# Kernel tuning notes

Hardware: AMD Instinct MI355X
Metric: run time of the kernel (lower is better)

The kernel has to match this reference:

```python
import jax, jax.numpy as jnp
import numpy as np

N = 50000      # nodes
E = 800000     # edges
IN = 64        # in_channels
HID = 256      # hidden_dim
LAT = 64       # latent_dim
KS = 2         # kernel_size per dim
DIM = 3        # pseudo-coordinate dim
K = KS ** DIM  # 8 spline weight matrices


def spline_basis_coeffs(pseudo, ks, dim, dtype):
    """Degree-1 open B-spline basis: returns per-edge coefficients c [E, ks**dim]."""
    e = pseudo.shape[0]
    v = pseudo * (ks - 1)                                   # [E, dim]
    bot = jnp.clip(jnp.floor(v), 0, ks - 1).astype(jnp.int32)
    frac = v - bot
    c = jnp.zeros((e, ks ** dim), dtype)
    rows = jnp.arange(e)
    for s in range(2 ** dim):  # 8 knot combinations (fixed small loop)
        w = jnp.ones(e, dtype)
        idx = jnp.zeros(e, jnp.int32)
        for d in range(dim):
            bit = (s >> d) & 1
            w = w * (frac[:, d] if bit else 1.0 - frac[:, d])
            idx = idx + jnp.clip(bot[:, d] + bit, 0, ks - 1) * (ks ** d)
        c = c.at[rows, idx].add(w)
    return c


def spline_conv(x, edge_index, pseudo, W, Wroot, b):
    """SplineConv with aggr='mean', root weight and bias (degree-1 open splines)."""
    src, dst = edge_index[0], edge_index[1]
    n = x.shape[0]
    e = pseudo.shape[0]
    c = spline_basis_coeffs(pseudo, KS, DIM, x.dtype)        # [E, K]
    x_src = x[src]                                           # [E, in] gather
    deg = jax.ops.segment_sum(jnp.ones(e, x.dtype), dst, num_segments=n)
    inv_deg = (1.0 / jnp.maximum(deg, 1.0))[:, None]         # [N, 1] mean aggr
    out = jnp.zeros((n, W.shape[2]), x.dtype)
    for k in range(W.shape[0]):  # K=8 fixed loop; scatter-add then dense matmul
        agg = jax.ops.segment_sum(c[:, k:k + 1] * x_src, dst, num_segments=n)
        out = out + (agg * inv_deg) @ W[k]
    return out + x @ Wroot + b


def setup_inputs() -> dict:
    key = jax.random.key(0)
    ks = jax.random.split(key, 12)
    x = jax.random.normal(ks[0], (N, IN), jnp.float32)
    edge_index = jax.random.randint(ks[1], (2, E), 0, N, jnp.int32)
    s = 0.05
    return {
        "x": x,
        "edge_index": edge_index,
        "conv1_W": jax.random.normal(ks[2], (K, IN, HID), jnp.float32) * s,
        "conv1_root": jax.random.normal(ks[3], (IN, HID), jnp.float32) * s,
        "conv1_b": jnp.zeros((HID,), jnp.float32),
        "conv2_W": jax.random.normal(ks[4], (K, HID, LAT), jnp.float32) * s,
        "conv2_root": jax.random.normal(ks[5], (HID, LAT), jnp.float32) * s,
        "conv2_b": jnp.zeros((LAT,), jnp.float32),
        "dec_w1": jax.random.normal(ks[6], (LAT, HID), jnp.float32) * s,
        "dec_b1": jnp.zeros((HID,), jnp.float32),
        "dec_w2": jax.random.normal(ks[7], (HID, IN), jnp.float32) * s,
        "dec_b2": jnp.zeros((IN,), jnp.float32),
    }


def reference(x, edge_index, conv1_W, conv1_root, conv1_b,
              conv2_W, conv2_root, conv2_b,
              dec_w1, dec_b1, dec_w2, dec_b2):
    pseudo = jnp.zeros((edge_index.shape[1], DIM), x.dtype)  # forward builds zeros
    h = jax.nn.relu(spline_conv(x, edge_index, pseudo, conv1_W, conv1_root, conv1_b))
    z = spline_conv(h, edge_index, pseudo, conv2_W, conv2_root, conv2_b)
    h2 = jax.nn.relu(z @ dec_w1 + dec_b1)
    return h2 @ dec_w2 + dec_b2
```

## Files before the change

kernel.cpp:

```cpp
#include <hip/hip_runtime.h>
#include <hip/hip_bf16.h>


#define THREADS 256

typedef __attribute__((ext_vector_type(8))) short bf16x8;
typedef __attribute__((ext_vector_type(4))) float f32x4;

__device__ __forceinline__ float bf2f(unsigned short u) {
    unsigned v = ((unsigned)u) << 16;
    return __builtin_bit_cast(float, v);
}
__device__ __forceinline__ unsigned short f2bf(float f) {
    __hip_bfloat16 h = __float2bfloat16(f);
    return __builtin_bit_cast(unsigned short, h);
}
__device__ __forceinline__ void acc8(float* f, uint4 v) {
    f[0] += bf2f((unsigned short)v.x); f[1] += bf2f((unsigned short)(v.x >> 16));
    f[2] += bf2f((unsigned short)v.y); f[3] += bf2f((unsigned short)(v.y >> 16));
    f[4] += bf2f((unsigned short)v.z); f[5] += bf2f((unsigned short)(v.z >> 16));
    f[6] += bf2f((unsigned short)v.w); f[7] += bf2f((unsigned short)(v.w >> 16));
}

__device__ __forceinline__ void pack_one(unsigned short* dst,
                                         const float* W0, const float* W1,
                                         int NB, int ksplit, int colsplit,
                                         int ld0, int ld1, int t) {
    int i = t & 7, lane = (t >> 3) & 63, rest = t >> 9;
    int j = rest % NB, s = rest / NB;
    int k = s * 32 + ((lane >> 4) << 3) + i;
    int c = (j << 4) + (lane & 15);
    float v;
    if (c >= colsplit)    v = W1[(size_t)k * ld1 + (c - colsplit)];
    else if (k >= ksplit) v = W1[(size_t)(k - ksplit) * ld1 + c];
    else                  v = W0[(size_t)k * ld0 + c];
    dst[t] = f2bf(v);
}

#define BIG (1 << 30)

__global__ void prep_kernel(const float* __restrict__ W1g, const float* __restrict__ root1,
                            const float* __restrict__ W2g, const float* __restrict__ root2,
                            const float* __restrict__ dw1, const float* __restrict__ dw2,
                            const float* __restrict__ x, const int* __restrict__ dstv,
                            int* __restrict__ bcnt,
                            unsigned short* __restrict__ Pb1,
                            unsigned short* __restrict__ Pb2,
                            unsigned short* __restrict__ Pd1,
                            unsigned short* __restrict__ Pd2,
                            unsigned short* __restrict__ ab1,
                            int n, int E, int pb_pack) {
    if ((int)blockIdx.x >= pb_pack) {
        __shared__ int hist[256];
        int t = threadIdx.x;
        hist[t] = 0;
        __syncthreads();
        int e0 = ((int)blockIdx.x - pb_pack) * 4096;
#pragma unroll
        for (int i = 0; i < 16; ++i) {
            int e = e0 + t + i * 256;
            if (e < E) atomicAdd(&hist[dstv[e] >> 8], 1);
        }
        __syncthreads();
        int h = hist[t];
        if (h) atomicAdd(&bcnt[t], h);
        return;
    }
    int t = blockIdx.x * blockDim.x + threadIdx.x;
    if (t < 32768) {
        pack_one(Pb1, W1g, root1, 16, 64, BIG, 256, 256, t);
    } else if (t < 65536) {
        pack_one(Pb2, W2g, root2, 8, BIG, 64, 64, 64, t - 32768);
    } else if (t < 81920) {
        pack_one(Pd1, dw1, dw1, 16, BIG, BIG, 256, 256, t - 65536);
    } else if (t < 98304) {
        pack_one(Pd2, dw2, dw2, 4, BIG, BIG, 64, 64, t - 81920);
    } else if (t < 98304 + n * 16) {
        int u = t - 98304;
        int row = u >> 4, c4 = (u & 15) * 4;
        float4 v = *(const float4*)(x + (size_t)row * 64 + c4);
        unsigned lo = (unsigned)f2bf(v.x) | ((unsigned)f2bf(v.y) << 16);
        unsigned hi = (unsigned)f2bf(v.z) | ((unsigned)f2bf(v.w) << 16);
        uint2 o; o.x = lo; o.y = hi;
        *(uint2*)(ab1 + (size_t)row * 128 + 64 + c4) = o;
    }
}

__global__ __launch_bounds__(512) void partition_edges(
    const int* __restrict__ src, const int* __restrict__ dst,
    const int* __restrict__ bcnt, int* __restrict__ bcur,
    int* __restrict__ epack, int E) {
    __shared__ int hist[256];
    __shared__ int base[256];
    __shared__ int lcur[256];
    __shared__ int bb[256];
    int t = threadIdx.x;
    if (t < 256) { hist[t] = 0; lcur[t] = 0; }
    __syncthreads();
    int e0 = blockIdx.x * 2048;
    int myd[4], mys[4];
#pragma unroll
    for (int i = 0; i < 4; ++i) {
        int e = e0 + t + i * 512;
        int d = (e < E) ? dst[e] : -1;
        mys[i] = (e < E) ? src[e] : 0;
        myd[i] = d;
        if (d >= 0) atomicAdd(&hist[d >> 8], 1);
    }
    int cb = 0;
    if (t < 256) { cb = bcnt[t]; bb[t] = cb; }
    __syncthreads();
    for (int off = 1; off < 256; off <<= 1) {
        int xv = (t >= off && t < 256) ? bb[t - off] : 0;
        __syncthreads();
        if (t < 256) bb[t] += xv;
        __syncthreads();
    }
    if (t < 256) {
        int h = hist[t];
        if (h > 0) base[t] = (bb[t] - cb) + atomicAdd(&bcur[t], h);
    }
    __syncthreads();
#pragma unroll
    for (int i = 0; i < 4; ++i) {
        int d = myd[i];
        if (d >= 0) {
            int b = d >> 8;
            int p = atomicAdd(&lcur[b], 1);
            epack[base[b] + p] = ((d & 255) << 20) | mys[i];
        }
    }
}

__global__ __launch_bounds__(1024) void bucket_fill2(
    const int* __restrict__ epack, const int* __restrict__ bcnt,
    int* __restrict__ offs, float* __restrict__ invd,
    int* __restrict__ esrc, int N) {
    __shared__ int sb_[256];
    __shared__ int nh[256];
    __shared__ int loff[256];
    __shared__ int ncur[256];
    __shared__ int stage[8192];
    int b = blockIdx.x, t = threadIdx.x;
    int n0 = b << 8;
    int cb = 0;
    if (t < 256) { cb = bcnt[t]; sb_[t] = cb; }
    __syncthreads();
    for (int off = 1; off < 256; off <<= 1) {
        int xv = (t >= off && t < 256) ? sb_[t - off] : 0;
        __syncthreads();
        if (t < 256) sb_[t] += xv;
        __syncthreads();
    }
    int ebase = b ? sb_[b - 1] : 0;
    int ecount = sb_[b] - ebase;
    if (b == 0 && t == 0) offs[N] = sb_[255];
    if (t < 256) nh[t] = 0;
    __syncthreads();
    for (int i = t; i < ecount; i += 1024)
        atomicAdd(&nh[epack[ebase + i] >> 20], 1);
    __syncthreads();
    int v = 0;
    if (t < 256) { v = nh[t]; loff[t] = v; }
    __syncthreads();
    for (int off = 1; off < 256; off <<= 1) {
        int xv = (t >= off && t < 256) ? loff[t - off] : 0;
        __syncthreads();
        if (t < 256) loff[t] += xv;
        __syncthreads();
    }
    if (t < 256) {
        int ex = loff[t] - v;
        loff[t] = ex;
        int node = n0 + t;
        if (node < N) {
            offs[node] = ebase + ex;
            invd[node] = 1.0f / (float)max(v, 1);
        }
        ncur[t] = 0;
    }
    __syncthreads();
    bool useLds = (ecount <= 8192);
    for (int i = t; i < ecount; i += 1024) {
        int p = epack[ebase + i];
        int dl = p >> 20;
        int pos = atomicAdd(&ncur[dl], 1);
        int g = loff[dl] + pos;
        int sv = p & 0xFFFFF;
        if (useLds) stage[g] = sv;
        else        esrc[ebase + g] = sv;
    }
    __syncthreads();
    if (useLds)
        for (int i = t; i < ecount; i += 1024) esrc[ebase + i] = stage[i];
}

__global__ void agg_x4(unsigned short* __restrict__ ab1, const int* __restrict__ esrc,
                       const int* __restrict__ offs, const float* __restrict__ invd,
                       int n) {
    int node = blockIdx.x * 4 + (threadIdx.x >> 6);
    if (node >= n) return;
    int l = threadIdx.x & 63;
    int slot = l >> 3, c = l & 7;
    const unsigned short* xb = ab1 + 64 + c * 8;
    int s = offs[node], e = offs[node + 1];
    float a0[8] = {}, a1[8] = {};
    int j = s;
    for (; j + 16 <= e; j += 16) {
        int i0 = esrc[j + slot], i1 = esrc[j + 8 + slot];
        uint4 v0 = *(const uint4*)(xb + (size_t)i0 * 128);
        uint4 v1 = *(const uint4*)(xb + (size_t)i1 * 128);
        acc8(a0, v0); acc8(a1, v1);
    }
    if (j + 8 <= e) {
        int i0 = esrc[j + slot];
        uint4 v0 = *(const uint4*)(xb + (size_t)i0 * 128);
        acc8(a0, v0);
        j += 8;
    }
    if (slot < e - j) {
        int i0 = esrc[j + slot];
        uint4 v0 = *(const uint4*)(xb + (size_t)i0 * 128);
        acc8(a1, v0);
    }
    float r[8];
#pragma unroll
    for (int k = 0; k < 8; ++k) {
        r[k] = a0[k] + a1[k];
        r[k] += __shfl_xor(r[k], 8);
        r[k] += __shfl_xor(r[k], 16);
        r[k] += __shfl_xor(r[k], 32);
    }
    if (slot == 0) {
        float iv = invd[node];
        unsigned p0 = (unsigned)f2bf(r[0] * iv) | ((unsigned)f2bf(r[1] * iv) << 16);
        unsigned p1 = (unsigned)f2bf(r[2] * iv) | ((unsigned)f2bf(r[3] * iv) << 16);
        unsigned p2 = (unsigned)f2bf(r[4] * iv) | ((unsigned)f2bf(r[5] * iv) << 16);
        unsigned p3 = (unsigned)f2bf(r[6] * iv) | ((unsigned)f2bf(r[7] * iv) << 16);
        uint4 o; o.x = p0; o.y = p1; o.z = p2; o.w = p3;
        *(uint4*)(ab1 + (size_t)node * 128 + c * 8) = o;
    }
}

__global__ void agg_z4(const unsigned short* __restrict__ hwroot,
                       const int* __restrict__ esrc, const int* __restrict__ offs,
                       const float* __restrict__ invd, const float* __restrict__ b2,
                       unsigned short* __restrict__ z, int n) {
    int node = blockIdx.x * 4 + (threadIdx.x >> 6);
    if (node >= n) return;
    int l = threadIdx.x & 63;
    int slot = l >> 3, c = l & 7;
    const unsigned short* hb = hwroot + c * 8;
    int s = offs[node], e = offs[node + 1];
    float a0[8] = {}, a1[8] = {};
    int j = s;
    for (; j + 16 <= e; j += 16) {
        int i0 = esrc[j + slot], i1 = esrc[j + 8 + slot];
        uint4 v0 = *(const uint4*)(hb + (size_t)i0 * 128);
        uint4 v1 = *(const uint4*)(hb + (size_t)i1 * 128);
        acc8(a0, v0); acc8(a1, v1);
    }
    if (j + 8 <= e) {
        int i0 = esrc[j + slot];
        uint4 v0 = *(const uint4*)(hb + (size_t)i0 * 128);
        acc8(a0, v0);
        j += 8;
    }
    if (slot < e - j) {
        int i0 = esrc[j + slot];
        uint4 v0 = *(const uint4*)(hb + (size_t)i0 * 128);
        acc8(a1, v0);
    }
    float r[8];
#pragma unroll
    for (int k = 0; k < 8; ++k) {
        r[k] = a0[k] + a1[k];
        r[k] += __shfl_xor(r[k], 8);
        r[k] += __shfl_xor(r[k], 16);
        r[k] += __shfl_xor(r[k], 32);
    }
    if (slot == 0) {
        float iv = invd[node];
        uint4 hr = *(const uint4*)(hwroot + (size_t)node * 128 + 64 + c * 8);
        float4 bA = *(const float4*)(b2 + c * 8);
        float4 bB = *(const float4*)(b2 + c * 8 + 4);
        float v0 = r[0] * iv + bf2f((unsigned short)hr.x) + bA.x;
        float v1 = r[1] * iv + bf2f((unsigned short)(hr.x >> 16)) + bA.y;
        float v2 = r[2] * iv + bf2f((unsigned short)hr.y) + bA.z;
        float v3 = r[3] * iv + bf2f((unsigned short)(hr.y >> 16)) + bA.w;
        float v4 = r[4] * iv + bf2f((unsigned short)hr.z) + bB.x;
        float v5 = r[5] * iv + bf2f((unsigned short)(hr.z >> 16)) + bB.y;
        float v6 = r[6] * iv + bf2f((unsigned short)hr.w) + bB.z;
        float v7 = r[7] * iv + bf2f((unsigned short)(hr.w >> 16)) + bB.w;
        unsigned p0 = (unsigned)f2bf(v0) | ((unsigned)f2bf(v1) << 16);
        unsigned p1 = (unsigned)f2bf(v2) | ((unsigned)f2bf(v3) << 16);
        unsigned p2 = (unsigned)f2bf(v4) | ((unsigned)f2bf(v5) << 16);
        unsigned p3 = (unsigned)f2bf(v6) | ((unsigned)f2bf(v7) << 16);
        uint4 o; o.x = p0; o.y = p1; o.z = p2; o.w = p3;
        *(uint4*)(z + (size_t)node * 64 + c * 8) = o;
    }
}

template <int K1, int NBW2, bool OUTBF>
__global__ __launch_bounds__(256) void gemm_fused(
    const unsigned short* __restrict__ A,
    const unsigned short* __restrict__ Bp1, const float* __restrict__ bias1,
    const unsigned short* __restrict__ Bp2, const float* __restrict__ bias2,
    void* __restrict__ Cv, int n)
{
    constexpr int KS1 = K1 / 32;
    constexpr int N2 = NBW2 * 64;
    constexpr int NB2 = NBW2 * 4;
    __shared__ unsigned short ht[64][264];

    const int m0 = blockIdx.x * 64;
    const int lane = threadIdx.x & 63;
    const int w = threadIdx.x >> 6;
    const int quad = lane >> 4;
    const int l16 = lane & 15;

    {
        f32x4 acc[4][4] = {};
        const unsigned short* Arow = A + (size_t)(m0 + l16) * K1 + quad * 8;
        for (int s = 0; s < KS1; ++s) {
            bf16x8 a[4];
#pragma unroll
            for (int mb = 0; mb < 4; ++mb)
                a[mb] = *(const bf16x8*)(Arow + (size_t)mb * 16 * K1 + s * 32);
#pragma unroll
            for (int jn = 0; jn < 4; ++jn) {
                int j = w * 4 + jn;
                bf16x8 b = *(const bf16x8*)(Bp1 + ((size_t)(s * 16 + j) * 64 + lane) * 8);
#pragma unroll
                for (int mb = 0; mb < 4; ++mb)
                    acc[mb][jn] = __builtin_amdgcn_mfma_f32_16x16x32_bf16(a[mb], b, acc[mb][jn], 0, 0, 0);
            }
        }
#pragma unroll
        for (int jn = 0; jn < 4; ++jn) {
            int col = (w * 4 + jn) * 16 + l16;
            float bv = bias1[col];
#pragma unroll
            for (int mb = 0; mb < 4; ++mb)
#pragma unroll
                for (int r = 0; r < 4; ++r) {
                    int row = mb * 16 + quad * 4 + r;
                    ht[row][col] = f2bf(fmaxf(acc[mb][jn][r] + bv, 0.f));
                }
        }
    }
    __syncthreads();

    {
        f32x4 acc[4][NBW2] = {};
        for (int s = 0; s < 8; ++s) {
            bf16x8 a[4];
#pragma unroll
            for (int mb = 0; mb < 4; ++mb)
                a[mb] = *(const bf16x8*)&ht[mb * 16 + l16][s * 32 + quad * 8];
#pragma unroll
            for (int jn = 0; jn < NBW2; ++jn) {
                int j = w * NBW2 + jn;
                bf16x8 b = *(const bf16x8*)(Bp2 + ((size_t)(s * NB2 + j) * 64 + lane) * 8);
#pragma unroll
                for (int mb = 0; mb < 4; ++mb)
                    acc[mb][jn] = __builtin_amdgcn_mfma_f32_16x16x32_bf16(a[mb], b, acc[mb][jn], 0, 0, 0);
            }
        }
#pragma unroll
        for (int jn = 0; jn < NBW2; ++jn) {
            int col = (w * NBW2 + jn) * 16 + l16;
            float bv = bias2 ? bias2[col] : 0.f;
#pragma unroll
            for (int mb = 0; mb < 4; ++mb)
#pragma unroll
                for (int r = 0; r < 4; ++r) {
                    int row = m0 + mb * 16 + quad * 4 + r;
                    if (row < n) {
                        float v = acc[mb][jn][r] + bv;
                        if (OUTBF)
                            ((unsigned short*)Cv)[(size_t)row * N2 + col] = f2bf(v);
                        else
                            ((float*)Cv)[(size_t)row * N2 + col] = v;
                    }
                }
        }
    }
}

extern "C" void kernel_launch(void* const* d_in, const int* in_sizes, int n_in,
                              void* d_out, int out_size, void* d_ws, size_t ws_size,
                              hipStream_t stream) {
    const float* x      = (const float*)d_in[0];
    const int*   ei     = (const int*)d_in[1];
    const float* W1g    = (const float*)d_in[2];
    const float* root1  = (const float*)d_in[3];
    const float* b1     = (const float*)d_in[4];
    const float* W2g    = (const float*)d_in[5];
    const float* root2  = (const float*)d_in[6];
    const float* b2     = (const float*)d_in[7];
    const float* dw1    = (const float*)d_in[8];
    const float* db1    = (const float*)d_in[9];
    const float* dw2    = (const float*)d_in[10];
    const float* db2    = (const float*)d_in[11];
    float* out = (float*)d_out;

    const int N = in_sizes[0] / 64;
    const int E = in_sizes[1] / 2;
    const int Npad = N + 64;
    const int* srcv = ei;
    const int* dstv = ei + E;

    char* ws = (char*)d_ws;
    auto alloc = [&](size_t bytes) -> void* {
        void* p = (void*)ws;
        ws += (bytes + 255) & ~(size_t)255;
        return p;
    };
    int*   bcnt   = (int*)alloc(1024);
    int*   bcur   = (int*)alloc(1024);
    int*   offs   = (int*)alloc((size_t)(N + 1) * 4);
    float* invd   = (float*)alloc((size_t)N * 4);
    int*   esrc   = (int*)alloc((size_t)E * 4);
    int*   epack  = (int*)alloc((size_t)E * 4);
    unsigned short* Pb1 = (unsigned short*)alloc(32768 * 2);
    unsigned short* Pb2 = (unsigned short*)alloc(32768 * 2);
    unsigned short* Pd1 = (unsigned short*)alloc(16384 * 2);
    unsigned short* Pd2 = (unsigned short*)alloc(16384 * 2);
    unsigned short* ab1    = (unsigned short*)alloc((size_t)Npad * 128 * 2);
    unsigned short* hwroot = (unsigned short*)alloc((size_t)Npad * 128 * 2);
    unsigned short* z      = (unsigned short*)alloc((size_t)Npad * 64 * 2);

    hipMemsetAsync(bcnt, 0, 2048, stream);

    int gb = (N + 63) / 64;
    int nbkt = (N + 255) / 256;
    int pa = (E + 4095) / 4096;
    int pa2 = (E + 2047) / 2048;
    int pb_pack = (98304 + N * 16 + THREADS - 1) / THREADS;

    prep_kernel<<<pb_pack + pa, THREADS, 0, stream>>>(
        W1g, root1, W2g, root2, dw1, dw2, x, dstv, bcnt,
        Pb1, Pb2, Pd1, Pd2, ab1, N, E, pb_pack);
    partition_edges<<<pa2, 512, 0, stream>>>(srcv, dstv, bcnt, bcur, epack, E);
    bucket_fill2<<<nbkt, 1024, 0, stream>>>(epack, bcnt, offs, invd, esrc, N);

    agg_x4<<<(N + 3) / 4, THREADS, 0, stream>>>(ab1, esrc, offs, invd, N);
    gemm_fused<128, 2, true><<<gb, 256, 0, stream>>>(ab1, Pb1, b1, Pb2, nullptr, hwroot, N);
    agg_z4<<<(N + 3) / 4, THREADS, 0, stream>>>(hwroot, esrc, offs, invd, b2, z, N);
    gemm_fused<64, 1, false><<<gb, 256, 0, stream>>>(z, Pd1, db1, Pd2, db2, out, N);
}
```

Measured before the change: 198.0 us.

## Split neighbor aggregation into per-feature-slice blocks for cache locality

Replaces the per-node aggregation kernels with a templated kernel in which each block handles one 16-byte feature slice (8 bf16 values) for 32 nodes. Consecutive blocks walk the same nodes across different slices, and each gather touches only one 16B slice of a 256B row. The intent is a smaller working set per slice so gathered rows stay in L2/MALL. Each wave now handles 4 nodes at once with 16 edge slots per node and a divergent __any loop. The histogram pass in prep also uses 2048-edge chunks to match partition_edges, adding more parallelism.

```diff
diff --git a/kernel.cpp b/kernel.cpp
--- a/kernel.cpp
+++ b/kernel.cpp
@@ -55,9 +55,9 @@
         int t = threadIdx.x;
         hist[t] = 0;
         __syncthreads();
-        int e0 = ((int)blockIdx.x - pb_pack) * 4096;
-#pragma unroll
-        for (int i = 0; i < 16; ++i) {
+        int e0 = ((int)blockIdx.x - pb_pack) * 2048;
+#pragma unroll
+        for (int i = 0; i < 8; ++i) {
             int e = e0 + t + i * 256;
             if (e < E) atomicAdd(&hist[dstv[e] >> 8], 1);
         }
@@ -195,109 +195,66 @@
         for (int i = t; i < ecount; i += 1024) esrc[ebase + i] = stage[i];
 }
 
-__global__ void agg_x4(unsigned short* __restrict__ ab1, const int* __restrict__ esrc,
-                       const int* __restrict__ offs, const float* __restrict__ invd,
-                       int n) {
-    int node = blockIdx.x * 4 + (threadIdx.x >> 6);
-    if (node >= n) return;
-    int l = threadIdx.x & 63;
-    int slot = l >> 3, c = l & 7;
-    const unsigned short* xb = ab1 + 64 + c * 8;
-    int s = offs[node], e = offs[node + 1];
-    float a0[8] = {}, a1[8] = {};
-    int j = s;
-    for (; j + 16 <= e; j += 16) {
-        int i0 = esrc[j + slot], i1 = esrc[j + 8 + slot];
-        uint4 v0 = *(const uint4*)(xb + (size_t)i0 * 128);
-        uint4 v1 = *(const uint4*)(xb + (size_t)i1 * 128);
-        acc8(a0, v0); acc8(a1, v1);
-    }
-    if (j + 8 <= e) {
-        int i0 = esrc[j + slot];
-        uint4 v0 = *(const uint4*)(xb + (size_t)i0 * 128);
-        acc8(a0, v0);
-        j += 8;
-    }
-    if (slot < e - j) {
-        int i0 = esrc[j + slot];
-        uint4 v0 = *(const uint4*)(xb + (size_t)i0 * 128);
-        acc8(a1, v0);
-    }
-    float r[8];
-#pragma unroll
-    for (int k = 0; k < 8; ++k) {
-        r[k] = a0[k] + a1[k];
-        r[k] += __shfl_xor(r[k], 8);
-        r[k] += __shfl_xor(r[k], 16);
-        r[k] += __shfl_xor(r[k], 32);
-    }
-    if (slot == 0) {
-        float iv = invd[node];
-        unsigned p0 = (unsigned)f2bf(r[0] * iv) | ((unsigned)f2bf(r[1] * iv) << 16);
-        unsigned p1 = (unsigned)f2bf(r[2] * iv) | ((unsigned)f2bf(r[3] * iv) << 16);
-        unsigned p2 = (unsigned)f2bf(r[4] * iv) | ((unsigned)f2bf(r[5] * iv) << 16);
-        unsigned p3 = (unsigned)f2bf(r[6] * iv) | ((unsigned)f2bf(r[7] * iv) << 16);
-        uint4 o; o.x = p0; o.y = p1; o.z = p2; o.w = p3;
-        *(uint4*)(ab1 + (size_t)node * 128 + c * 8) = o;
-    }
-}
-
-__global__ void agg_z4(const unsigned short* __restrict__ hwroot,
-                       const int* __restrict__ esrc, const int* __restrict__ offs,
-                       const float* __restrict__ invd, const float* __restrict__ b2,
-                       unsigned short* __restrict__ z, int n) {
-    int node = blockIdx.x * 4 + (threadIdx.x >> 6);
-    if (node >= n) return;
-    int l = threadIdx.x & 63;
-    int slot = l >> 3, c = l & 7;
-    const unsigned short* hb = hwroot + c * 8;
-    int s = offs[node], e = offs[node + 1];
-    float a0[8] = {}, a1[8] = {};
-    int j = s;
-    for (; j + 16 <= e; j += 16) {
-        int i0 = esrc[j + slot], i1 = esrc[j + 8 + slot];
-        uint4 v0 = *(const uint4*)(hb + (size_t)i0 * 128);
-        uint4 v1 = *(const uint4*)(hb + (size_t)i1 * 128);
-        acc8(a0, v0); acc8(a1, v1);
-    }
-    if (j + 8 <= e) {
-        int i0 = esrc[j + slot];
-        uint4 v0 = *(const uint4*)(hb + (size_t)i0 * 128);
-        acc8(a0, v0);
-        j += 8;
-    }
-    if (slot < e - j) {
-        int i0 = esrc[j + slot];
-        uint4 v0 = *(const uint4*)(hb + (size_t)i0 * 128);
-        acc8(a1, v0);
-    }
-    float r[8];
-#pragma unroll
-    for (int k = 0; k < 8; ++k) {
-        r[k] = a0[k] + a1[k];
-        r[k] += __shfl_xor(r[k], 8);
-        r[k] += __shfl_xor(r[k], 16);
-        r[k] += __shfl_xor(r[k], 32);
-    }
-    if (slot == 0) {
-        float iv = invd[node];
-        uint4 hr = *(const uint4*)(hwroot + (size_t)node * 128 + 64 + c * 8);
-        float4 bA = *(const float4*)(b2 + c * 8);
-        float4 bB = *(const float4*)(b2 + c * 8 + 4);
-        float v0 = r[0] * iv + bf2f((unsigned short)hr.x) + bA.x;
-        float v1 = r[1] * iv + bf2f((unsigned short)(hr.x >> 16)) + bA.y;
-        float v2 = r[2] * iv + bf2f((unsigned short)hr.y) + bA.z;
-        float v3 = r[3] * iv + bf2f((unsigned short)(hr.y >> 16)) + bA.w;
-        float v4 = r[4] * iv + bf2f((unsigned short)hr.z) + bB.x;
-        float v5 = r[5] * iv + bf2f((unsigned short)(hr.z >> 16)) + bB.y;
-        float v6 = r[6] * iv + bf2f((unsigned short)hr.w) + bB.z;
-        float v7 = r[7] * iv + bf2f((unsigned short)(hr.w >> 16)) + bB.w;
-        unsigned p0 = (unsigned)f2bf(v0) | ((unsigned)f2bf(v1) << 16);
-        unsigned p1 = (unsigned)f2bf(v2) | ((unsigned)f2bf(v3) << 16);
-        unsigned p2 = (unsigned)f2bf(v4) | ((unsigned)f2bf(v5) << 16);
-        unsigned p3 = (unsigned)f2bf(v6) | ((unsigned)f2bf(v7) << 16);
-        uint4 o; o.x = p0; o.y = p1; o.z = p2; o.w = p3;
-        *(uint4*)(z + (size_t)node * 64 + c * 8) = o;
+template <int MODE>
+__global__ __launch_bounds__(256) void agg_slice(
+    const unsigned short* __restrict__ tbl,
+    const int* __restrict__ esrc, const int* __restrict__ offs,
+    const float* __restrict__ invd, const float* __restrict__ b2,
+    const unsigned short* __restrict__ hwroot,
+    unsigned short* __restrict__ outb, int n) {
+    const int b = blockIdx.x;
+    const int s = b & 7, grp = b >> 3;
+    const int l = threadIdx.x & 63, w = threadIdx.x >> 6;
+    const int nsub = l & 3, slot = l >> 2;
+    const int OS = (MODE == 0) ? 128 : 64;
+    const unsigned short* tb = tbl + ((MODE == 0) ? 64 : 0) + s * 8;
+
+#pragma unroll
+    for (int q = 0; q < 2; ++q) {
+        int node = grp * 32 + w * 8 + q * 4 + nsub;
+        bool valid = node < n;
+        int s0 = valid ? offs[node] : 0;
+        int e0 = valid ? offs[node + 1] : 0;
+        float a[8] = {};
+        int j = s0 + slot;
+        while (__any(j < e0)) {
+            if (j < e0) {
+                int src = esrc[j];
+                uint4 v = *(const uint4*)(tb + (size_t)src * 128);
+                acc8(a, v);
+            }
+            j += 16;
+        }
+#pragma unroll
+        for (int k = 0; k < 8; ++k) {
+            a[k] += __shfl_xor(a[k], 4);
+            a[k] += __shfl_xor(a[k], 8);
+            a[k] += __shfl_xor(a[k], 16);
+            a[k] += __shfl_xor(a[k], 32);
+        }
+        if (slot == 0 && valid) {
+            float iv = invd[node];
+            float v[8];
+#pragma unroll
+            for (int k = 0; k < 8; ++k) v[k] = a[k] * iv;
+            if (MODE == 1) {
+                uint4 hr = *(const uint4*)(hwroot + (size_t)node * 128 + 64 + s * 8);
+                v[0] += bf2f((unsigned short)hr.x)         + b2[s * 8 + 0];
+                v[1] += bf2f((unsigned short)(hr.x >> 16)) + b2[s * 8 + 1];
+                v[2] += bf2f((unsigned short)hr.y)         + b2[s * 8 + 2];
+                v[3] += bf2f((unsigned short)(hr.y >> 16)) + b2[s * 8 + 3];
+                v[4] += bf2f((unsigned short)hr.z)         + b2[s * 8 + 4];
+                v[5] += bf2f((unsigned short)(hr.z >> 16)) + b2[s * 8 + 5];
+                v[6] += bf2f((unsigned short)hr.w)         + b2[s * 8 + 6];
+                v[7] += bf2f((unsigned short)(hr.w >> 16)) + b2[s * 8 + 7];
+            }
+            unsigned p0 = (unsigned)f2bf(v[0]) | ((unsigned)f2bf(v[1]) << 16);
+            unsigned p1 = (unsigned)f2bf(v[2]) | ((unsigned)f2bf(v[3]) << 16);
+            unsigned p2 = (unsigned)f2bf(v[4]) | ((unsigned)f2bf(v[5]) << 16);
+            unsigned p3 = (unsigned)f2bf(v[6]) | ((unsigned)f2bf(v[7]) << 16);
+            uint4 o; o.x = p0; o.y = p1; o.z = p2; o.w = p3;
+            *(uint4*)(outb + (size_t)node * OS + s * 8) = o;
+        }
     }
 }
 
@@ -435,18 +392,20 @@
 
     int gb = (N + 63) / 64;
     int nbkt = (N + 255) / 256;
-    int pa = (E + 4095) / 4096;
-    int pa2 = (E + 2047) / 2048;
+    int pa = (E + 2047) / 2048;
     int pb_pack = (98304 + N * 16 + THREADS - 1) / THREADS;
+    int ga = ((N + 31) / 32) * 8;
 
     prep_kernel<<<pb_pack + pa, THREADS, 0, stream>>>(
         W1g, root1, W2g, root2, dw1, dw2, x, dstv, bcnt,
         Pb1, Pb2, Pd1, Pd2, ab1, N, E, pb_pack);
-    partition_edges<<<pa2, 512, 0, stream>>>(srcv, dstv, bcnt, bcur, epack, E);
+    partition_edges<<<pa, 512, 0, stream>>>(srcv, dstv, bcnt, bcur, epack, E);
     bucket_fill2<<<nbkt, 1024, 0, stream>>>(epack, bcnt, offs, invd, esrc, N);
 
-    agg_x4<<<(N + 3) / 4, THREADS, 0, stream>>>(ab1, esrc, offs, invd, N);
+    agg_slice<0><<<ga, THREADS, 0, stream>>>(ab1, esrc, offs, invd, nullptr,
+                                             nullptr, ab1, N);
     gemm_fused<128, 2, true><<<gb, 256, 0, stream>>>(ab1, Pb1, b1, Pb2, nullptr, hwroot, N);
-    agg_z4<<<(N + 3) / 4, THREADS, 0, stream>>>(hwroot, esrc, offs, invd, b2, z, N);
+    agg_slice<1><<<ga, THREADS, 0, stream>>>(hwroot, esrc, offs, invd, b2,
+                                             hwroot, z, N);
     gemm_fused<64, 1, false><<<gb, 256, 0, stream>>>(z, Pd1, db1, Pd2, db2, out, N);
 }
```

Result: slower. 297.4 us (+50.2%).

## Split LDS histograms into four sub-bins and reuse atomic ranks for scatter

Applied to the files above, without the earlier changes.

The bucket histograms in prep, partition and bucket_fill are spread across four sub-bins per bucket, picked by lane index, so fewer lanes contend on the same LDS atomic. The rank returned by the first atomic is kept and combined with a scan over the sub-bins to place each edge directly. This replaces the second atomic pass and the LDS staging buffer. In exchange it adds a 1024-entry prefix scan per block and more LDS use, and the esrc writes become scattered global stores rather than a coalesced copy from LDS.

```diff
diff --git a/kernel.cpp b/kernel.cpp
--- a/kernel.cpp
+++ b/kernel.cpp
@@ -51,18 +51,19 @@
                             unsigned short* __restrict__ ab1,
                             int n, int E, int pb_pack) {
     if ((int)blockIdx.x >= pb_pack) {
-        __shared__ int hist[256];
+        __shared__ int hist[1024];
         int t = threadIdx.x;
-        hist[t] = 0;
+        hist[t] = 0; hist[t + 256] = 0; hist[t + 512] = 0; hist[t + 768] = 0;
         __syncthreads();
         int e0 = ((int)blockIdx.x - pb_pack) * 4096;
+        int sub = t & 3;
 #pragma unroll
         for (int i = 0; i < 16; ++i) {
             int e = e0 + t + i * 256;
-            if (e < E) atomicAdd(&hist[dstv[e] >> 8], 1);
-        }
-        __syncthreads();
-        int h = hist[t];
+            if (e < E) atomicAdd(&hist[((dstv[e] >> 8) << 2) | sub], 1);
+        }
+        __syncthreads();
+        int h = hist[t * 4] + hist[t * 4 + 1] + hist[t * 4 + 2] + hist[t * 4 + 3];
         if (h) atomicAdd(&bcnt[t], h);
         return;
     }
@@ -90,22 +91,33 @@
     const int* __restrict__ src, const int* __restrict__ dst,
     const int* __restrict__ bcnt, int* __restrict__ bcur,
     int* __restrict__ epack, int E) {
-    __shared__ int hist[256];
+    __shared__ int h4[1024];
+    __shared__ int s4[1024];
     __shared__ int base[256];
-    __shared__ int lcur[256];
     __shared__ int bb[256];
     int t = threadIdx.x;
-    if (t < 256) { hist[t] = 0; lcur[t] = 0; }
+    h4[t] = 0; h4[t + 512] = 0;
     __syncthreads();
     int e0 = blockIdx.x * 2048;
-    int myd[4], mys[4];
+    int sub = t & 3;
+    int myd[4], mys[4], myr[4];
 #pragma unroll
     for (int i = 0; i < 4; ++i) {
         int e = e0 + t + i * 512;
         int d = (e < E) ? dst[e] : -1;
         mys[i] = (e < E) ? src[e] : 0;
         myd[i] = d;
-        if (d >= 0) atomicAdd(&hist[d >> 8], 1);
+        if (d >= 0) myr[i] = atomicAdd(&h4[((d >> 8) << 2) | sub], 1);
+    }
+    __syncthreads();
+    s4[t] = h4[t]; s4[t + 512] = h4[t + 512];
+    __syncthreads();
+    for (int off = 1; off < 1024; off <<= 1) {
+        int v0 = (t >= off) ? s4[t - off] : 0;
+        int v1 = (t + 512 >= off) ? s4[t + 512 - off] : 0;
+        __syncthreads();
+        s4[t] += v0; s4[t + 512] += v1;
+        __syncthreads();
     }
     int cb = 0;
     if (t < 256) { cb = bcnt[t]; bb[t] = cb; }
@@ -117,8 +129,10 @@
         __syncthreads();
     }
     if (t < 256) {
-        int h = hist[t];
-        if (h > 0) base[t] = (bb[t] - cb) + atomicAdd(&bcur[t], h);
+        int lo = t ? s4[t * 4 - 1] : 0;
+        int h = s4[t * 4 + 3] - lo;
+        if (h > 0)
+            base[t] = (bb[t] - cb) + atomicAdd(&bcur[t], h) - lo;
     }
     __syncthreads();
 #pragma unroll
@@ -126,8 +140,9 @@
         int d = myd[i];
         if (d >= 0) {
             int b = d >> 8;
-            int p = atomicAdd(&lcur[b], 1);
-            epack[base[b] + p] = ((d & 255) << 20) | mys[i];
+            int flat = (b << 2) | sub;
+            int pre = flat ? s4[flat - 1] : 0;
+            epack[base[b] + pre + myr[i]] = ((d & 255) << 20) | mys[i];
         }
     }
 }
@@ -137,10 +152,9 @@
     int* __restrict__ offs, float* __restrict__ invd,
     int* __restrict__ esrc, int N) {
     __shared__ int sb_[256];
-    __shared__ int nh[256];
-    __shared__ int loff[256];
+    __shared__ int n4[1024];
     __shared__ int ncur[256];
-    __shared__ int stage[8192];
+    __shared__ int rk[8192];
     int b = blockIdx.x, t = threadIdx.x;
     int n0 = b << 8;
     int cb = 0;
@@ -155,44 +169,50 @@
     int ebase = b ? sb_[b - 1] : 0;
     int ecount = sb_[b] - ebase;
     if (b == 0 && t == 0) offs[N] = sb_[255];
-    if (t < 256) nh[t] = 0;
-    __syncthreads();
-    for (int i = t; i < ecount; i += 1024)
-        atomicAdd(&nh[epack[ebase + i] >> 20], 1);
-    __syncthreads();
-    int v = 0;
-    if (t < 256) { v = nh[t]; loff[t] = v; }
-    __syncthreads();
-    for (int off = 1; off < 256; off <<= 1) {
-        int xv = (t >= off && t < 256) ? loff[t - off] : 0;
-        __syncthreads();
-        if (t < 256) loff[t] += xv;
+    n4[t] = 0;
+    __syncthreads();
+    bool useRk = (ecount <= 8192);
+    int sub = t & 3;
+    for (int i = t; i < ecount; i += 1024) {
+        int dl = epack[ebase + i] >> 20;
+        int r = atomicAdd(&n4[(dl << 2) | sub], 1);
+        if (useRk) rk[i] = r;
+    }
+    __syncthreads();
+    for (int off = 1; off < 1024; off <<= 1) {
+        int xv = (t >= off) ? n4[t - off] : 0;
+        __syncthreads();
+        n4[t] += xv;
         __syncthreads();
     }
     if (t < 256) {
-        int ex = loff[t] - v;
-        loff[t] = ex;
+        int lo = t ? n4[t * 4 - 1] : 0;
+        int v = n4[t * 4 + 3] - lo;
         int node = n0 + t;
         if (node < N) {
-            offs[node] = ebase + ex;
+            offs[node] = ebase + lo;
             invd[node] = 1.0f / (float)max(v, 1);
         }
         ncur[t] = 0;
     }
     __syncthreads();
-    bool useLds = (ecount <= 8192);
-    for (int i = t; i < ecount; i += 1024) {
-        int p = epack[ebase + i];
-        int dl = p >> 20;
-        int pos = atomicAdd(&ncur[dl], 1);
-        int g = loff[dl] + pos;
-        int sv = p & 0xFFFFF;
-        if (useLds) stage[g] = sv;
-        else        esrc[ebase + g] = sv;
-    }
-    __syncthreads();
-    if (useLds)
-        for (int i = t; i < ecount; i += 1024) esrc[ebase + i] = stage[i];
+    if (useRk) {
+        for (int i = t; i < ecount; i += 1024) {
+            int p = epack[ebase + i];
+            int dl = p >> 20;
+            int flat = (dl << 2) | (i & 3);
+            int pre = flat ? n4[flat - 1] : 0;
+            esrc[ebase + pre + rk[i]] = p & 0xFFFFF;
+        }
+    } else {
+        for (int i = t; i < ecount; i += 1024) {
+            int p = epack[ebase + i];
+            int dl = p >> 20;
+            int lo = dl ? n4[dl * 4 - 1] : 0;
+            int pos = atomicAdd(&ncur[dl], 1);
+            esrc[ebase + lo + pos] = p & 0xFFFFF;
+        }
+    }
 }
 
 __global__ void agg_x4(unsigned short* __restrict__ ab1, const int* __restrict__ esrc,
```

Measured after the change: 203.2 us. 1.03x slower.
